# Kernel optimization log

Measured on AMD Instinct MI355X. Metric: run time of the kernel, lower is better.

## Reference

```python
import jax, jax.numpy as jnp
import numpy as np
from jax import lax

K2 = 3                 # support_kernel_size
TARGET_OCC = 0.5
OCC_W = 10.0
ITERS = 10             # flood-fill iterations
THRESH = 0.5
STEEP = 20.0

# 6-neighbor 3D cross kernel (plus-shaped), shape [O=1, I=1, 3, 3, 3]
_cross_np = np.zeros((1, 1, 3, 3, 3), dtype=np.float32)
for dz, dy, dx in [(0, 1, 1), (2, 1, 1), (1, 0, 1), (1, 2, 1), (1, 1, 0), (1, 1, 2)]:
    _cross_np[0, 0, dz, dy, dx] = 1.0


def _conv3d(x, k, pad):
    # x: [B, C, D, H, W], k: [O, I, kd, kh, kw]
    return lax.conv_general_dilated(
        x, k, window_strides=(1, 1, 1), padding=pad,
        dimension_numbers=('NCDHW', 'OIDHW', 'NCDHW'))


def setup_inputs() -> dict:
    key = jax.random.key(0)
    voxel_grid = jax.random.uniform(key, (4, 1, 128, 128, 128), dtype=jnp.float32)
    return {"voxel_grid": voxel_grid}


def reference(voxel_grid):
    B, C, D, H, W = voxel_grid.shape
    N = B * D * H * W
    dt = voxel_grid.dtype

    # ---- overhang score: vectorized over all z-slices at once ----
    # per-slice conv2d(3x3 ones) == conv3d with kernel depth 1
    k2 = jnp.ones((1, 1, 1, K2, K2), dt)
    below = voxel_grid[:, :, :-1]          # [B,1,D-1,H,W]
    curr = voxel_grid[:, :, 1:]
    below_support = _conv3d(below, k2, ((0, 0), (1, 1), (1, 1)))
    support_ratio = below_support / (K2 * K2)
    overhang = (curr * (1.0 - support_ratio)).sum() / N

    # ---- surface area score ----
    k3 = jnp.ones((1, 1, 3, 3, 3), dt)
    neighbor_solid = _conv3d(voxel_grid, k3, ((1, 1), (1, 1), (1, 1)))
    surface_term = neighbor_solid.sum() / 27.0 / N

    occupancy = voxel_grid.sum() / N
    occupancy_penalty = OCC_W * (occupancy - TARGET_OCC) ** 2

    # differentiable flood-fill (diff_find_enclosed_voids)
    seed = jnp.zeros_like(voxel_grid).at[:, :, 5, 5, 5].set(1.0)
    cross = jnp.asarray(_cross_np, dt)
    not_solid = 1.0 - voxel_grid

    def body(i, mask):
        c = _conv3d(mask, cross, ((1, 1), (1, 1), (1, 1)))
        act = jax.nn.sigmoid(STEEP * (c - THRESH))
        return jnp.maximum(mask, act) * not_solid

    enclosed = lax.fori_loop(0, ITERS, body, seed)
    resin_trap_penalty = 100.0 * enclosed.sum() / N

    surface_score = surface_term - resin_trap_penalty - occupancy_penalty
    return overhang, surface_score
```

## Files before the change

kernel.cpp:

```cpp
#include <hip/hip_runtime.h>

#define HW    (128*128)
#define DHW   (128*128*128)
#define NTOT  (4*DHW)
#define NBLK  8192

__device__ __forceinline__ float sigf(float x){ return 1.0f/(1.0f+__expf(-x)); }
__device__ __forceinline__ float4 ld4(const float* p){ return *(const float4*)p; }


__global__ __launch_bounds__(256, 4) void mega_k(
    const float* __restrict__ v, float* __restrict__ p_occ,
    float* __restrict__ p_surf, float* __restrict__ p_over,
    float* __restrict__ p_trap)
{
    __shared__ float4 smem4[1445];
    __shared__ float sred[16];
    float* smem = (float*)smem4;

    const int bid = blockIdx.x;
    const int tid = threadIdx.x;

    if (bid < 4) {
        const int b = bid;
        const size_t gb = (size_t)b * DHW;
        const int ty = tid & 15, tz = tid >> 4;
        const float a_lo = sigf(-10.0f), a_hi = sigf(10.0f);
        const float4 zero4 = make_float4(0,0,0,0);
        #define M(zz,yy) (smem + (((zz)*17 + (yy))*20))

        float m[16], nv[16];
        {
            const float* rv = v + gb + ((size_t)tz*128 + ty)*128;
            int dzy = abs(tz-5) + abs(ty-5);
            #pragma unroll
            for (int q = 0; q < 4; ++q) {
                int x4 = 4*q;
                float4 a = ld4(rv + x4);
                nv[x4+0]=1.f-a.x; nv[x4+1]=1.f-a.y; nv[x4+2]=1.f-a.z; nv[x4+3]=1.f-a.w;
                int d0=dzy+abs(x4+0-5), d1=dzy+abs(x4+1-5);
                int d2=dzy+abs(x4+2-5), d3=dzy+abs(x4+3-5);
                m[x4+0] = ((d0==0)?1.f:((d0==1)?a_hi:a_lo)) * nv[x4+0];
                m[x4+1] = ((d1==0)?1.f:((d1==1)?a_hi:a_lo)) * nv[x4+1];
                m[x4+2] = ((d2==0)?1.f:((d2==1)?a_hi:a_lo)) * nv[x4+2];
                m[x4+3] = ((d3==0)?1.f:((d3==1)?a_hi:a_lo)) * nv[x4+3];
                *(float4*)(M(tz,ty) + x4) = make_float4(m[x4+0],m[x4+1],m[x4+2],m[x4+3]);
            }
        }
        const float xrE = a_lo * (1.f - v[gb + ((size_t)tz*128 + ty)*128 + 16]);
        {
            int a = tid >> 4, e = tid & 15;
            M(16,a)[e] = a_lo * (1.f - v[gb + ((size_t)16*128 + a)*128 + e]);
            M(a,16)[e] = a_lo * (1.f - v[gb + ((size_t)a*128 + 16)*128 + e]);
        }
        __syncthreads();

        for (int it = 0; it < 9; ++it) {
            const float* YM = M(tz,ty-1);
            const float* YP = M(tz,ty+1);
            const float* ZM = M(tz-1,ty);
            const float* ZP = M(tz+1,ty);
            float nm[16];
            #pragma unroll
            for (int q = 0; q < 4; ++q) {
                int x4 = 4*q;
                float4 ym = (ty > 0) ? *(const float4*)(YM + x4) : zero4;
                float4 yp = *(const float4*)(YP + x4);
                float4 zm = (tz > 0) ? *(const float4*)(ZM + x4) : zero4;
                float4 zp = *(const float4*)(ZP + x4);
                float xl = (q == 0) ? 0.f : m[x4-1];
                float xr = (q == 3) ? xrE : m[x4+4];
                float s0 = xl      + m[x4+1] + ym.x + yp.x + zm.x + zp.x;
                float s1 = m[x4+0] + m[x4+2] + ym.y + yp.y + zm.y + zp.y;
                float s2 = m[x4+1] + m[x4+3] + ym.z + yp.z + zm.z + zp.z;
                float s3 = m[x4+2] + xr      + ym.w + yp.w + zm.w + zp.w;
                nm[x4+0] = fmaxf(m[x4+0], sigf(20.f*s0 - 10.f)) * nv[x4+0];
                nm[x4+1] = fmaxf(m[x4+1], sigf(20.f*s1 - 10.f)) * nv[x4+1];
                nm[x4+2] = fmaxf(m[x4+2], sigf(20.f*s2 - 10.f)) * nv[x4+2];
                nm[x4+3] = fmaxf(m[x4+3], sigf(20.f*s3 - 10.f)) * nv[x4+3];
            }
            __syncthreads();
            float* W = M(tz,ty);
            #pragma unroll
            for (int q = 0; q < 4; ++q) {
                int x4 = 4*q;
                *(float4*)(W + x4) = make_float4(nm[x4+0],nm[x4+1],nm[x4+2],nm[x4+3]);
                m[x4+0]=nm[x4+0]; m[x4+1]=nm[x4+1]; m[x4+2]=nm[x4+2]; m[x4+3]=nm[x4+3];
            }
            __syncthreads();
        }

        float d = 0.f;
        #pragma unroll
        for (int x = 0; x < 16; ++x) d += m[x] - a_lo * nv[x];
        #pragma unroll
        for (int o = 32; o; o >>= 1) d += __shfl_down(d, o, 64);
        int lane = tid & 63, wid = tid >> 6;
        if (lane == 0) sred[wid] = d;
        __syncthreads();
        if (tid == 0) p_trap[b] = sred[0] + sred[1] + sred[2] + sred[3];
        #undef M
    } else {
        const int rid = bid - 4;
        const int b   = rid >> 11;
        const int rem = rid & 2047;
        const int z   = rem >> 4;
        const int y0  = (rem & 15) * 8;
        const int tx  = tid & 31, ty = tid >> 5;
        const int y   = y0 + ty;
        const int x4  = tx * 4;
        const size_t idx = (size_t)b*DHW + ((size_t)z*128 + y)*128 + x4;
        #define ROWS(r) (smem + (r)*132)

        if (z >= 1) {
            const float* bp = v + (size_t)b*DHW + (size_t)(z-1)*HW;
            const float4 zero = make_float4(0,0,0,0);
            for (int i = tid; i < 320; i += 256) {
                int r = i >> 5, q = (i & 31)*4;
                int gy = y0 - 1 + r;
                float4 qv = ((unsigned)gy <= 127u) ? ld4(bp + (size_t)gy*128 + q) : zero;
                *(float4*)(ROWS(r) + q) = qv;
            }
            if (tid < 20) ROWS(tid>>1)[130 + (tid&1)] = 0.f;
        }
        __syncthreads();

        float4 val = ld4(v + idx);
        float occ = val.x + val.y + val.z + val.w;

        float wz = (z==0 || z==127) ? 2.f : 3.f;
        float wy = (y==0 || y==127) ? 2.f : 3.f;
        float wx0 = (x4==0)   ? 2.f : 3.f;
        float wx3 = (x4==124) ? 2.f : 3.f;
        float surf = wz*wy*(wx0*val.x + 3.f*val.y + 3.f*val.z + wx3*val.w);

        float over = 0.f;
        if (z >= 1) {
            float sx=0, sy=0, szz=0, sw=0;
            #pragma unroll
            for (int dy = 0; dy < 3; ++dy) {
                const float* R = ROWS(ty + dy);
                float4 q = *(const float4*)(R + x4);
                float ql = R[(tx==0)  ? 130 : x4-1];
                float qr = R[(tx==31) ? 131 : x4+4];
                sx  += ql  + q.x + q.y;
                sy  += q.x + q.y + q.z;
                szz += q.y + q.z + q.w;
                sw  += q.z + q.w + qr;
            }
            const float inv9 = 1.f/9.f;
            over = val.x*(1.f - sx*inv9) + val.y*(1.f - sy*inv9)
                 + val.z*(1.f - szz*inv9) + val.w*(1.f - sw*inv9);
        }

        #pragma unroll
        for (int o = 32; o; o >>= 1) {
            occ  += __shfl_down(occ,  o, 64);
            surf += __shfl_down(surf, o, 64);
            over += __shfl_down(over, o, 64);
        }
        int lane = tid & 63, wid = tid >> 6;
        if (lane == 0) { sred[wid]=occ; sred[4+wid]=surf; sred[8+wid]=over; }
        __syncthreads();
        if (tid == 0) {
            p_occ [rid] = sred[0]+sred[1]+sred[2]+sred[3];
            p_surf[rid] = sred[4]+sred[5]+sred[6]+sred[7];
            p_over[rid] = sred[8]+sred[9]+sred[10]+sred[11];
        }
        #undef ROWS
    }
}

__global__ __launch_bounds__(1024) void finalize_k(
    const float* __restrict__ p_occ, const float* __restrict__ p_surf,
    const float* __restrict__ p_over, const float* __restrict__ p_trap,
    float* __restrict__ out)
{
    double occ=0, surf=0, over=0;
    for (int i = threadIdx.x; i < NBLK; i += 1024) {
        occ += p_occ[i]; surf += p_surf[i]; over += p_over[i];
    }
    __shared__ double sm[3][16];
    #pragma unroll
    for (int o = 32; o; o >>= 1) {
        occ  += __shfl_down(occ,  o, 64);
        surf += __shfl_down(surf, o, 64);
        over += __shfl_down(over, o, 64);
    }
    int lane = threadIdx.x & 63, wid = threadIdx.x >> 6;
    if (lane == 0) { sm[0][wid]=occ; sm[1][wid]=surf; sm[2][wid]=over; }
    __syncthreads();
    if (threadIdx.x == 0) {
        double so=0, ss=0, sv=0;
        for (int w = 0; w < 16; ++w) { so+=sm[0][w]; ss+=sm[1][w]; sv+=sm[2][w]; }
        double dS = (double)p_trap[0] + p_trap[1] + p_trap[2] + p_trap[3];
        double a_lo = 1.0 / (1.0 + exp(10.0));
        double N = (double)NTOT;
        double trap_sum = a_lo * (N - so) + dS;
        double occupancy = so / N;
        double occ_pen = 10.0 * (occupancy - 0.5) * (occupancy - 0.5);
        out[0] = (float)(sv / N);
        out[1] = (float)(ss / 27.0 / N - 100.0 * trap_sum / N - occ_pen);
    }
}

extern "C" void kernel_launch(void* const* d_in, const int* in_sizes, int n_in,
                              void* d_out, int out_size, void* d_ws, size_t ws_size,
                              hipStream_t stream)
{
    const float* v = (const float*)d_in[0];
    float* out = (float*)d_out;
    float* ws = (float*)d_ws;

    float* p_occ  = ws;
    float* p_surf = p_occ  + NBLK;
    float* p_over = p_surf + NBLK;
    float* p_trap = p_over + NBLK;

    mega_k<<<NBLK + 4, 256, 0, stream>>>(v, p_occ, p_surf, p_over, p_trap);
    finalize_k<<<1, 1024, 0, stream>>>(p_occ, p_surf, p_over, p_trap, out);
}
```

Baseline: 89.23 us.

## Process four z-slices per block, reusing each slice as the next one's support plane

Each reduction block now walks four consecutive z-slices instead of one, cutting the block count from 8192 to 2048. Each slice it has already loaded becomes the 'below' plane for the next slice. The horizontal 3-tap sums are precomputed with wavefront shuffles and stored in a double-buffered shared-memory tile, so only the two halo rows are fetched from global memory. This aims to cut redundant global reads of the below slice and repeated stencil arithmetic, at the cost of extra barriers per slice and less block-level parallelism.

```diff
diff --git a/kernel.cpp b/kernel.cpp
--- a/kernel.cpp
+++ b/kernel.cpp
@@ -3,7 +3,7 @@
 #define HW    (128*128)
 #define DHW   (128*128*128)
 #define NTOT  (4*DHW)
-#define NBLK  8192
+#define NBLK  2048
 
 __device__ __forceinline__ float sigf(float x){ return 1.0f/(1.0f+__expf(-x)); }
 __device__ __forceinline__ float4 ld4(const float* p){ return *(const float4*)p; }
@@ -20,13 +20,13 @@
 
     const int bid = blockIdx.x;
     const int tid = threadIdx.x;
+    const float4 zero4 = make_float4(0,0,0,0);
 
     if (bid < 4) {
         const int b = bid;
         const size_t gb = (size_t)b * DHW;
         const int ty = tid & 15, tz = tid >> 4;
         const float a_lo = sigf(-10.0f), a_hi = sigf(10.0f);
-        const float4 zero4 = make_float4(0,0,0,0);
         #define M(zz,yy) (smem + (((zz)*17 + (yy))*20))
 
         float m[16], nv[16];
@@ -102,55 +102,75 @@
         #undef M
     } else {
         const int rid = bid - 4;
-        const int b   = rid >> 11;
-        const int rem = rid & 2047;
-        const int z   = rem >> 4;
+        const int b   = rid >> 9;
+        const int rem = rid & 511;
+        const int z0  = (rem >> 4) * 4;
         const int y0  = (rem & 15) * 8;
         const int tx  = tid & 31, ty = tid >> 5;
+        const int x4  = tx * 4;
         const int y   = y0 + ty;
-        const int x4  = tx * 4;
-        const size_t idx = (size_t)b*DHW + ((size_t)z*128 + y)*128 + x4;
-        #define ROWS(r) (smem + (r)*132)
-
-        if (z >= 1) {
-            const float* bp = v + (size_t)b*DHW + (size_t)(z-1)*HW;
-            const float4 zero = make_float4(0,0,0,0);
+        const size_t gb = (size_t)b * DHW;
+        #define PB(p,r) (smem + ((p)*1320 + (r)*132))
+
+        float occ = 0.f, surf = 0.f, over = 0.f;
+
+        if (z0 >= 1) {
+            const float* bp = v + gb + (size_t)(z0-1)*HW;
             for (int i = tid; i < 320; i += 256) {
-                int r = i >> 5, q = (i & 31)*4;
+                int r = i >> 5, xq = i & 31, xi = xq*4;
                 int gy = y0 - 1 + r;
-                float4 qv = ((unsigned)gy <= 127u) ? ld4(bp + (size_t)gy*128 + q) : zero;
-                *(float4*)(ROWS(r) + q) = qv;
-            }
-            if (tid < 20) ROWS(tid>>1)[130 + (tid&1)] = 0.f;
-        }
-        __syncthreads();
-
-        float4 val = ld4(v + idx);
-        float occ = val.x + val.y + val.z + val.w;
-
-        float wz = (z==0 || z==127) ? 2.f : 3.f;
-        float wy = (y==0 || y==127) ? 2.f : 3.f;
-        float wx0 = (x4==0)   ? 2.f : 3.f;
-        float wx3 = (x4==124) ? 2.f : 3.f;
-        float surf = wz*wy*(wx0*val.x + 3.f*val.y + 3.f*val.z + wx3*val.w);
-
-        float over = 0.f;
-        if (z >= 1) {
-            float sx=0, sy=0, szz=0, sw=0;
-            #pragma unroll
-            for (int dy = 0; dy < 3; ++dy) {
-                const float* R = ROWS(ty + dy);
-                float4 q = *(const float4*)(R + x4);
-                float ql = R[(tx==0)  ? 130 : x4-1];
-                float qr = R[(tx==31) ? 131 : x4+4];
-                sx  += ql  + q.x + q.y;
-                sy  += q.x + q.y + q.z;
-                szz += q.y + q.z + q.w;
-                sw  += q.z + q.w + qr;
-            }
-            const float inv9 = 1.f/9.f;
-            over = val.x*(1.f - sx*inv9) + val.y*(1.f - sy*inv9)
-                 + val.z*(1.f - szz*inv9) + val.w*(1.f - sw*inv9);
+                float4 q = ((unsigned)gy <= 127u) ? ld4(bp + gy*128 + xi) : zero4;
+                float ql = __shfl_up(q.w, 1);   if (xq == 0)  ql = 0.f;
+                float qr = __shfl_down(q.x, 1); if (xq == 31) qr = 0.f;
+                *(float4*)(PB(0,r) + xi) =
+                    make_float4(ql+q.x+q.y, q.x+q.y+q.z, q.y+q.z+q.w, q.z+q.w+qr);
+            }
+        }
+        __syncthreads();
+
+        const float wy = (y==0 || y==127) ? 2.f : 3.f;
+        const float wx0 = (x4==0)   ? 2.f : 3.f;
+        const float wx3 = (x4==124) ? 2.f : 3.f;
+        const float inv9 = 1.f/9.f;
+
+        int pb = 0;
+        for (int s = 0; s < 4; ++s) {
+            const int z = z0 + s;
+            const float* cp = v + gb + (size_t)z*HW;
+            float4 val = ld4(cp + y*128 + x4);
+
+            occ += val.x + val.y + val.z + val.w;
+            float wz = (z==0 || z==127) ? 2.f : 3.f;
+            surf += wz*wy*(wx0*val.x + 3.f*val.y + 3.f*val.z + wx3*val.w);
+
+            if (z >= 1) {
+                float4 a = *(const float4*)(PB(pb, ty)   + x4);
+                float4 c = *(const float4*)(PB(pb, ty+1) + x4);
+                float4 d = *(const float4*)(PB(pb, ty+2) + x4);
+                float4 S = make_float4(a.x+c.x+d.x, a.y+c.y+d.y,
+                                       a.z+c.z+d.z, a.w+c.w+d.w);
+                over += val.x*(1.f - S.x*inv9) + val.y*(1.f - S.y*inv9)
+                      + val.z*(1.f - S.z*inv9) + val.w*(1.f - S.w*inv9);
+            }
+
+            if (s < 3) {
+                float ql = __shfl_up(val.w, 1);   if (tx == 0)  ql = 0.f;
+                float qr = __shfl_down(val.x, 1); if (tx == 31) qr = 0.f;
+                *(float4*)(PB(pb^1, ty+1) + x4) =
+                    make_float4(ql+val.x+val.y, val.x+val.y+val.z,
+                                val.y+val.z+val.w, val.z+val.w+qr);
+                if (tid < 64) {
+                    int h = tid >> 5, xq = tid & 31, xi = xq*4;
+                    int gy = h ? (y0 + 8) : (y0 - 1);
+                    float4 q = ((unsigned)gy <= 127u) ? ld4(cp + gy*128 + xi) : zero4;
+                    float hl = __shfl_up(q.w, 1);   if (xq == 0)  hl = 0.f;
+                    float hr = __shfl_down(q.x, 1); if (xq == 31) hr = 0.f;
+                    *(float4*)(PB(pb^1, h*9) + xi) =
+                        make_float4(hl+q.x+q.y, q.x+q.y+q.z, q.y+q.z+q.w, q.z+q.w+hr);
+                }
+                pb ^= 1;
+            }
+            __syncthreads();
         }
 
         #pragma unroll
@@ -167,7 +187,7 @@
             p_surf[rid] = sred[4]+sred[5]+sred[6]+sred[7];
             p_over[rid] = sred[8]+sred[9]+sred[10]+sred[11];
         }
-        #undef ROWS
+        #undef PB
     }
 }
 
```

Result: faster. 84.49 us (-5.3%).
